# Kernel tuning notes

Hardware: AMD Instinct MI355X
Metric: run time of the kernel (lower is better)

## Reference

```python
import jax, jax.numpy as jnp
import numpy as np
from jax.scipy.special import erf

# ---- problem constants (mirror module __init__ / placedb) ----
NUM_NODES = 2_000_000
NUM_FLOPS = 800_000
XL, YL, XH, YH = 0.0, 0.0, 168.0, 480.0
SX, SY = 1.0, 1.0                 # inst_stddev_x/y; bin pitch == stddev
INV_SX, INV_SY = 1.0 / SX, 1.0 / SY
TRUNC = 2.5
EXT = max(round(TRUNC - 0.5), 0)  # = 2 -> 5x5 smear window
NBX, NBY, NCK, NCE = 168, 480, 8, 8
CAP = 16                          # SLICE_CAPACITY (UltraScale: 16 FF/slice)
INST_AREA = SX * SY               # kernel receives inst_stddev_x*inst_stddev_y
INV_SQRT2 = 1.0 / np.sqrt(2.0)


def setup_inputs() -> dict:
    key = jax.random.key(0)
    k1, k2, k3, k4, k5 = jax.random.split(key, 5)
    x = jax.random.uniform(k1, (NUM_NODES,), minval=XL, maxval=XH, dtype=jnp.float32)
    y = jax.random.uniform(k2, (NUM_NODES,), minval=YL, maxval=YH, dtype=jnp.float32)
    pos = jnp.concatenate([x, y])  # [2*num_nodes]: x block then y block
    node_size_x = jax.random.uniform(k3, (NUM_NODES,), minval=0.1, maxval=1.0, dtype=jnp.float32)
    node_size_y = jax.random.uniform(k4, (NUM_NODES,), minval=0.1, maxval=1.0, dtype=jnp.float32)
    flop_indices = (jnp.arange(NUM_FLOPS, dtype=jnp.int32) * 2)  # unique, in-range
    flop_ctrlSets = jax.random.randint(k5, (NUM_FLOPS, 2), 0, NCK, dtype=jnp.int32)  # (ck, ce)
    return {"pos": pos, "node_size_x": node_size_x, "node_size_y": node_size_y,
            "flop_indices": flop_indices, "flop_ctrlSets": flop_ctrlSets}


def _smear_1d(centers, bin0, nbins, lo_edge, stddev, inv_std):
    """Gaussian integral over each bin in the truncated window. -> bins [F,W], dem [F,W]."""
    offs = jnp.arange(-EXT, EXT + 1, dtype=jnp.int32)
    b = bin0[:, None] + offs[None, :]
    valid = (b >= 0) & (b < nbins)
    bc = jnp.clip(b, 0, nbins - 1)
    lo = lo_edge + bc.astype(centers.dtype) * stddev
    s = inv_std * INV_SQRT2
    dem = 0.5 * (erf((lo + stddev - centers[:, None]) * s) - erf((lo - centers[:, None]) * s))
    return bc, jnp.where(valid, dem, jnp.zeros_like(dem))


def reference(pos, node_size_x, node_size_y, flop_indices, flop_ctrlSets):
    fi = flop_indices.astype(jnp.int32)
    ck = flop_ctrlSets[:, 0].astype(jnp.int32)
    ce = flop_ctrlSets[:, 1].astype(jnp.int32)

    # instance centers
    cx = pos[fi] + 0.5 * node_size_x[fi]
    cy = pos[NUM_NODES + fi] + 0.5 * node_size_y[fi]

    bx0 = jnp.clip(jnp.floor((cx - XL) * INV_SX).astype(jnp.int32), 0, NBX - 1)
    by0 = jnp.clip(jnp.floor((cy - YL) * INV_SY).astype(jnp.int32), 0, NBY - 1)

    bx, demx = _smear_1d(cx, bx0, NBX, XL, SX, INV_SX)  # [F, 5]
    by, demy = _smear_1d(cy, by0, NBY, YL, SY, INV_SY)  # [F, 5]

    # Gaussian-smeared demand contributions [F, 5, 5]
    dem = (INST_AREA * demx[:, :, None] * demy[:, None, :]).astype(pos.dtype)
    # flattened 4D bin index (x, y, ck, ce)
    idx = ((bx[:, :, None] * NBY + by[:, None, :]) * NCK + ck[:, None, None]) * NCE + ce[:, None, None]

    dem_map = jnp.zeros(NBX * NBY * NCK * NCE, dtype=pos.dtype)
    dem_map = dem_map.at[idx.reshape(-1)].add(dem.reshape(-1))
    dem_map = dem_map.reshape(NBX, NBY, NCK, NCE)

    # HALF ctrl mode slice quantization (UltraScale): quarter=CAP/4 FFs share CE,
    # half = 2 quarters share CK/SR, slice = 2 halves.
    quarters = jnp.sum(jnp.ceil(dem_map / (CAP // 4)), axis=3)   # [x,y,ck]
    halves = jnp.sum(jnp.ceil(0.5 * quarters), axis=2)          # [x,y]
    slices = jnp.ceil(0.5 * halves)                             # [x,y]

    tot = dem_map.sum(axis=(2, 3))                              # [x,y]
    scale = jnp.where(tot > 0, slices * CAP / jnp.maximum(tot, 1e-12), jnp.zeros_like(tot))

    # gather quantized area back at each flop's center bin
    areas = INST_AREA * scale[bx0, by0]
    resource_areas = jnp.zeros(NUM_NODES, dtype=pos.dtype).at[fi].set(areas)
    return resource_areas / CAP
```

## Files before the change

### kernel.cpp

```cpp
#include <hip/hip_runtime.h>
#include <math.h>

#define NUM_NODES 2000000
#define NUM_FLOPS 800000
#define NBX 168
#define NBY 480
#define NCK 8
#define NCE 8
#define NBINS (NBX * NBY)
#define YB_ROWS 10
#define NYB 48
#define NBUCK (NYB * NBX)
#define CAPB 210
#define W 4
#define TILE_F (YB_ROWS * W * 64)
#define S_INVSQRT2 0.7071067811865476f
#define FILL_THREADS (784 * 1024)


struct Rec12 { float cx, cy; int keby; };

__device__ __forceinline__ float fast_erf(float x) {
    float ax = fabsf(x);
    float t = __builtin_amdgcn_rcpf(fmaf(0.3275911f, ax, 1.0f));
    float p = t * fmaf(t, fmaf(t, fmaf(t, fmaf(t, 1.061405429f, -1.453152027f),
                                       1.421413741f), -0.284496736f), 0.254829592f);
    float r = fmaf(-p, __expf(-ax * ax), 1.0f);
    return copysignf(r, x);
}

__global__ void __launch_bounds__(1024)
ff_fill(const float* __restrict__ pos,
        const float* __restrict__ nsx,
        const float* __restrict__ nsy,
        const int* __restrict__ fi,
        const int* __restrict__ cs,
        int* __restrict__ cnt,
        Rec12* __restrict__ rec,
        float* __restrict__ out) {
    __shared__ int h[NBUCK];
    __shared__ int base[NBUCK];
    int tid = threadIdx.x;
    int f = blockIdx.x * blockDim.x + tid;

    for (int g = f; g < NUM_NODES; g += FILL_THREADS) out[g] = 0.f;

    for (int j = tid; j < NBUCK; j += 1024) h[j] = 0;
    __syncthreads();

    bool valid = (f < NUM_FLOPS);
    int b1 = 0, b2 = -1, r1 = 0, r2 = 0, keby = 0;
    float cx = 0.f, cy = 0.f;
    if (valid) {
        int i = fi[f];
        cx = pos[i] + 0.5f * nsx[i];
        cy = pos[NUM_NODES + i] + 0.5f * nsy[i];
        int bx0 = (int)floorf(cx); bx0 = bx0 < 0 ? 0 : (bx0 > NBX - 1 ? NBX - 1 : bx0);
        int by0 = (int)floorf(cy); by0 = by0 < 0 ? 0 : (by0 > NBY - 1 ? NBY - 1 : by0);
        int2 cc = ((const int2*)cs)[f];
        keby = (by0 << 6) | (cc.x * NCE + cc.y);
        int yb = by0 / YB_ROWS;
        int rlo = by0 - yb * YB_ROWS;
        b1 = yb * NBX + bx0;
        r1 = atomicAdd(&h[b1], 1);
        if (rlo <= 1 && yb > 0)                       b2 = b1 - NBX;
        else if (rlo >= YB_ROWS - 2 && yb < NYB - 1)  b2 = b1 + NBX;
        if (b2 >= 0) r2 = atomicAdd(&h[b2], 1);
    }
    __syncthreads();
    for (int j = tid; j < NBUCK; j += 1024)
        base[j] = h[j] ? atomicAdd(&cnt[j], h[j]) : 0;
    __syncthreads();
    if (valid) {
        Rec12 v; v.cx = cx; v.cy = cy; v.keby = keby;
        int s1 = base[b1] + r1;
        if (s1 < CAPB) rec[(size_t)b1 * CAPB + s1] = v;
        if (b2 >= 0) {
            int s2 = base[b2] + r2;
            if (s2 < CAPB) rec[(size_t)b2 * CAPB + s2] = v;
        }
    }
}

__global__ void __launch_bounds__(256, 4)
ff_main(const int* __restrict__ cnt,
        const Rec12* __restrict__ rec,
        float* __restrict__ scale) {
    __shared__ __align__(16) float sh[4 * TILE_F];
    int tid = threadIdx.x;
    int wv = tid >> 6, lane = tid & 63;
    float* wtile = sh + wv * TILE_F;
    int c0 = blockIdx.x * W;
    int yb = blockIdx.y;
    int y0 = yb * YB_ROWS;

    for (int j = tid; j < TILE_F; j += 256)
        ((float4*)sh)[j] = make_float4(0.f, 0.f, 0.f, 0.f);
    __syncthreads();

    int c_lo = c0 - 2 < 0 ? 0 : c0 - 2;
    int c_hi = c0 + W + 1 > NBX - 1 ? NBX - 1 : c0 + W + 1;
    int nb = c_hi - c_lo + 1;
    int start[9];
    start[0] = 0;
#pragma unroll
    for (int k = 0; k < 8; ++k) {
        int n = 0;
        if (k < nb) { n = cnt[yb * NBX + c_lo + k]; n = n < CAPB ? n : CAPB; }
        start[k + 1] = start[k] + n;
    }
    int tot = start[8];
    const Rec12* bb = rec + (size_t)(yb * NBX + c_lo) * CAPB;

    for (int idx = tid; idx < tot; idx += 256) {
        int k = 0, off = idx;
#pragma unroll
        for (int t = 1; t < 8; ++t) { bool g = idx >= start[t]; k = g ? t : k; off = g ? idx - start[t] : off; }
        Rec12 v = bb[(size_t)k * CAPB + off];
        float cx = v.cx, cy = v.cy;
        int ke  = v.keby & 63;
        int by0 = v.keby >> 6;
        int bx0 = c_lo + k;
        float ex[W + 1], ey[6];
#pragma unroll
        for (int i = 0; i <= W; ++i)
            ex[i] = fast_erf(((float)(c0 + i) - cx) * S_INVSQRT2);
#pragma unroll
        for (int j = 0; j < 6; ++j)
            ey[j] = fast_erf(((float)(by0 - 2 + j) - cy) * S_INVSQRT2);
        float dyq[5];
#pragma unroll
        for (int j = 0; j < 5; ++j) dyq[j] = ey[j + 1] - ey[j];
        float dxq[W];
        int cmask = 0;
#pragma unroll
        for (int i = 0; i < W; ++i) {
            int col = c0 + i;
            dxq[i] = 0.25f * (ex[i + 1] - ex[i]);
            cmask |= (col >= bx0 - 2 && col <= bx0 + 2) ? (1 << i) : 0;
        }
        int r0 = by0 - 2 - y0;

        unsigned long long peers = __ballot(1);
#pragma unroll
        for (int b = 0; b < 6; ++b) {
            unsigned long long bl = __ballot((ke >> b) & 1);
            peers &= ((ke >> b) & 1) ? bl : ~bl;
        }
        int rank = (int)__popcll(peers & ((1ull << lane) - 1ull));

        for (int r = 0;; ++r) {
            if (!__ballot(rank == r)) break;
            if (rank == r) {
#pragma unroll
                for (int i = 0; i < W; ++i) {
                    if (cmask & (1 << i)) {
#pragma unroll
                        for (int j = 0; j < 5; ++j) {
                            int rl = r0 + j;
                            if ((unsigned)rl < YB_ROWS)
                                wtile[rl * (W * 64) + i * 64 + ke] += dxq[i] * dyq[j];
                        }
                    }
                }
            }
            asm volatile("s_waitcnt lgkmcnt(0)" ::: "memory");
        }
    }
    __syncthreads();

    if (tid < YB_ROWS * W) {
        int rl = tid >> 2, cl = tid & 3;
        int off = rl * (W * 64) + cl * 64;
        float tot2 = 0.f, halves = 0.f;
#pragma unroll
        for (int ck = 0; ck < NCK; ++ck) {
            float q = 0.f;
#pragma unroll
            for (int h2 = 0; h2 < 2; ++h2) {
                float4 d = make_float4(0.f, 0.f, 0.f, 0.f);
#pragma unroll
                for (int w2 = 0; w2 < 4; ++w2) {
                    float4 e = *(const float4*)(sh + w2 * TILE_F + off + ck * 8 + h2 * 4);
                    d.x += e.x; d.y += e.y; d.z += e.z; d.w += e.w;
                }
                tot2 += d.x + d.y + d.z + d.w;
                q += ceilf(d.x * 0.25f) + ceilf(d.y * 0.25f) +
                     ceilf(d.z * 0.25f) + ceilf(d.w * 0.25f);
            }
            halves += ceilf(0.5f * q);
        }
        float slices = ceilf(0.5f * halves);
        scale[(c0 + cl) * NBY + y0 + rl] = (tot2 > 0.f) ? (slices / fmaxf(tot2, 1e-12f)) : 0.f;
    }
}

__global__ void ff_gather(const float* __restrict__ pos,
                          const float* __restrict__ nsx,
                          const float* __restrict__ nsy,
                          const int* __restrict__ fi,
                          const float* __restrict__ scale,
                          float* __restrict__ out) {
    int f = blockIdx.x * blockDim.x + threadIdx.x;
    if (f >= NUM_FLOPS) return;
    int i = fi[f];
    float cx = pos[i] + 0.5f * nsx[i];
    float cy = pos[NUM_NODES + i] + 0.5f * nsy[i];
    int bx0 = (int)floorf(cx); bx0 = bx0 < 0 ? 0 : (bx0 > NBX - 1 ? NBX - 1 : bx0);
    int by0 = (int)floorf(cy); by0 = by0 < 0 ? 0 : (by0 > NBY - 1 ? NBY - 1 : by0);
    out[i] = scale[bx0 * NBY + by0];
}

extern "C" void kernel_launch(void* const* d_in, const int* in_sizes, int n_in,
                              void* d_out, int out_size, void* d_ws, size_t ws_size,
                              hipStream_t stream) {
    const float* pos = (const float*)d_in[0];
    const float* nsx = (const float*)d_in[1];
    const float* nsy = (const float*)d_in[2];
    const int*   fi  = (const int*)d_in[3];
    const int*   cs  = (const int*)d_in[4];
    float* out = (float*)d_out;

    float* scale = (float*)d_ws;
    int*   cnt   = (int*)(scale + NBINS);
    Rec12* rec   = (Rec12*)(scale + NBINS + NBUCK);

    hipMemsetAsync(cnt, 0, NBUCK * sizeof(int), stream);

    ff_fill<<<784, 1024, 0, stream>>>(pos, nsx, nsy, fi, cs, cnt, rec, out);
    ff_main<<<dim3(NBX / W, NYB), 256, 0, stream>>>(cnt, rec, scale);
    ff_gather<<<(NUM_FLOPS + 255) / 256, 256, 0, stream>>>(pos, nsx, nsy, fi, scale, out);
}
```

Measured before the change: 188.1 us.

## Narrow column tile to two and pad LDS tile rows for branch-free accumulation

Halves the bucket-column tile width per block from four to two. It adds four halo rows on each side of the per-wave LDS tile, so every flop's 5x2 contribution is written with unconditional load-FMA-store sequences. Column validity becomes a multiplicative mask instead of per-element branches and row bounds checks. The cost is that each record is now read and run through erf by more blocks (six source columns per two output columns), and twice as many blocks are launched.

```diff
diff --git a/kernel.cpp b/kernel.cpp
--- a/kernel.cpp
+++ b/kernel.cpp
@@ -12,8 +12,9 @@
 #define NYB 48
 #define NBUCK (NYB * NBX)
 #define CAPB 210
-#define W 4
-#define TILE_F (YB_ROWS * W * 64)
+#define W 2
+#define TROWS (YB_ROWS + 8)
+#define TILE_F (TROWS * W * 64)
 #define S_INVSQRT2 0.7071067811865476f
 #define FILL_THREADS (784 * 1024)
 
@@ -101,21 +102,21 @@
     int c_lo = c0 - 2 < 0 ? 0 : c0 - 2;
     int c_hi = c0 + W + 1 > NBX - 1 ? NBX - 1 : c0 + W + 1;
     int nb = c_hi - c_lo + 1;
-    int start[9];
+    int start[7];
     start[0] = 0;
 #pragma unroll
-    for (int k = 0; k < 8; ++k) {
+    for (int k = 0; k < 6; ++k) {
         int n = 0;
         if (k < nb) { n = cnt[yb * NBX + c_lo + k]; n = n < CAPB ? n : CAPB; }
         start[k + 1] = start[k] + n;
     }
-    int tot = start[8];
+    int tot = start[6];
     const Rec12* bb = rec + (size_t)(yb * NBX + c_lo) * CAPB;
 
     for (int idx = tid; idx < tot; idx += 256) {
         int k = 0, off = idx;
 #pragma unroll
-        for (int t = 1; t < 8; ++t) { bool g = idx >= start[t]; k = g ? t : k; off = g ? idx - start[t] : off; }
+        for (int t = 1; t < 6; ++t) { bool g = idx >= start[t]; k = g ? t : k; off = g ? idx - start[t] : off; }
         Rec12 v = bb[(size_t)k * CAPB + off];
         float cx = v.cx, cy = v.cy;
         int ke  = v.keby & 63;
@@ -132,14 +133,13 @@
 #pragma unroll
         for (int j = 0; j < 5; ++j) dyq[j] = ey[j + 1] - ey[j];
         float dxq[W];
-        int cmask = 0;
 #pragma unroll
         for (int i = 0; i < W; ++i) {
             int col = c0 + i;
-            dxq[i] = 0.25f * (ex[i + 1] - ex[i]);
-            cmask |= (col >= bx0 - 2 && col <= bx0 + 2) ? (1 << i) : 0;
-        }
-        int r0 = by0 - 2 - y0;
+            float m = (col >= bx0 - 2 && col <= bx0 + 2) ? 1.f : 0.f;
+            dxq[i] = 0.25f * (ex[i + 1] - ex[i]) * m;
+        }
+        int rr0 = by0 - y0 + 2;
 
         unsigned long long peers = __ballot(1);
 #pragma unroll
@@ -152,17 +152,20 @@
         for (int r = 0;; ++r) {
             if (!__ballot(rank == r)) break;
             if (rank == r) {
-#pragma unroll
-                for (int i = 0; i < W; ++i) {
-                    if (cmask & (1 << i)) {
-#pragma unroll
-                        for (int j = 0; j < 5; ++j) {
-                            int rl = r0 + j;
-                            if ((unsigned)rl < YB_ROWS)
-                                wtile[rl * (W * 64) + i * 64 + ke] += dxq[i] * dyq[j];
-                        }
-                    }
-                }
+                float* t0 = wtile + rr0 * (W * 64) + ke;
+                float a0 = t0[0 * 128], a1 = t0[1 * 128], a2 = t0[2 * 128],
+                      a3 = t0[3 * 128], a4 = t0[4 * 128];
+                float b0 = t0[0 * 128 + 64], b1 = t0[1 * 128 + 64], b2 = t0[2 * 128 + 64],
+                      b3 = t0[3 * 128 + 64], b4 = t0[4 * 128 + 64];
+                a0 = fmaf(dxq[0], dyq[0], a0); b0 = fmaf(dxq[1], dyq[0], b0);
+                a1 = fmaf(dxq[0], dyq[1], a1); b1 = fmaf(dxq[1], dyq[1], b1);
+                a2 = fmaf(dxq[0], dyq[2], a2); b2 = fmaf(dxq[1], dyq[2], b2);
+                a3 = fmaf(dxq[0], dyq[3], a3); b3 = fmaf(dxq[1], dyq[3], b3);
+                a4 = fmaf(dxq[0], dyq[4], a4); b4 = fmaf(dxq[1], dyq[4], b4);
+                t0[0 * 128] = a0; t0[1 * 128] = a1; t0[2 * 128] = a2;
+                t0[3 * 128] = a3; t0[4 * 128] = a4;
+                t0[0 * 128 + 64] = b0; t0[1 * 128 + 64] = b1; t0[2 * 128 + 64] = b2;
+                t0[3 * 128 + 64] = b3; t0[4 * 128 + 64] = b4;
             }
             asm volatile("s_waitcnt lgkmcnt(0)" ::: "memory");
         }
@@ -170,8 +173,8 @@
     __syncthreads();
 
     if (tid < YB_ROWS * W) {
-        int rl = tid >> 2, cl = tid & 3;
-        int off = rl * (W * 64) + cl * 64;
+        int rl = tid >> 1, cl = tid & 1;
+        int off = (rl + 4) * (W * 64) + cl * 64;
         float tot2 = 0.f, halves = 0.f;
 #pragma unroll
         for (int ck = 0; ck < NCK; ++ck) {
```

Result: no change. 187.7 us (-0.2%).
